# Performance work log

Hardware: AMD Instinct MI355X
Metric: run time of the kernel (lower is better)

## Reference

```python
import jax, jax.numpy as jnp
import numpy as np

GRID_SIZE = 5
SPLINE_ORDER = 3
EPS = 1e-5


def make_grid(in_features):
    # efficient-kan: grid_range=[-1,1], points from -order..grid_size+order
    h = 2.0 / GRID_SIZE
    g = jnp.arange(-SPLINE_ORDER, GRID_SIZE + SPLINE_ORDER + 1, dtype=jnp.float32) * h - 1.0
    return jnp.tile(g[None, :], (in_features, 1))  # [in, grid_size + 2*order + 1]


def b_splines(x, grid):
    # x: [B, in], grid: [in, G] -> bases: [B, in, grid_size + order]
    xg = x[:, :, None]
    bases = ((xg >= grid[:, :-1]) & (xg < grid[:, 1:])).astype(x.dtype)
    for k in range(1, SPLINE_ORDER + 1):
        left = (xg - grid[:, : -(k + 1)]) / (grid[:, k:-1] - grid[:, : -(k + 1)])
        right = (grid[:, k + 1:] - xg) / (grid[:, k + 1:] - grid[:, 1:-k])
        bases = left * bases[:, :, :-1] + right * bases[:, :, 1:]
    return bases


def kan_linear(x, grid, base_w, spline_w, spline_scaler):
    # base path: silu(x) @ base_w.T ; spline path: bsplines(x) contracted with scaled spline weight
    base_out = jnp.einsum('bi,oi->bo', jax.nn.silu(x), base_w)
    bases = b_splines(x, grid)  # [B, in, C]
    sw = spline_w * spline_scaler[:, :, None]  # [out, in, C]
    spline_out = jnp.einsum('bic,oic->bo', bases, sw)
    return base_out + spline_out


def layer_norm(x, w, b):
    mu = jnp.mean(x, axis=-1, keepdims=True)
    var = jnp.mean(jnp.square(x - mu), axis=-1, keepdims=True)
    return (x - mu) * jax.lax.rsqrt(var + EPS) * w + b


def setup_inputs() -> dict:
    key = jax.random.key(0)
    ks = jax.random.split(key, 8)
    B, F, H, E = 65536, 32, 64, 64
    OUT = E * F  # 2048
    C = GRID_SIZE + SPLINE_ORDER  # 8 coeffs per edge
    x = jax.random.normal(ks[0], (B, F), dtype=jnp.float32)
    return {
        'x': x,
        'ln_w': jnp.ones((F,), jnp.float32),
        'ln_b': jnp.zeros((F,), jnp.float32),
        'bw1': jax.random.normal(ks[1], (H, F), jnp.float32) * 0.1,
        'sw1': jax.random.normal(ks[2], (H, F, C), jnp.float32) * 0.1,
        'ss1': jax.random.normal(ks[3], (H, F), jnp.float32) * 0.1 + 1.0,
        'bw2': jax.random.normal(ks[4], (OUT, H), jnp.float32) * 0.1,
        'sw2': jax.random.normal(ks[5], (OUT, H, C), jnp.float32) * 0.1,
        'ss2': jax.random.normal(ks[6], (OUT, H), jnp.float32) * 0.1 + 1.0,
        'grid1': make_grid(F),
        'grid2': make_grid(H),
    }


def reference(x, ln_w, ln_b, bw1, sw1, ss1, bw2, sw2, ss2, grid1, grid2):
    h = layer_norm(x, ln_w, ln_b)
    h = kan_linear(h, grid1, bw1, sw1, ss1)   # [B, 64]
    out = kan_linear(h, grid2, bw2, sw2, ss2)  # [B, 2048]
    return out
```

## Files before the change

kernel.cpp:

```cpp
#include <hip/hip_runtime.h>
#include <stdint.h>

#define BATCH   65536
#define FIN     32
#define HID     64
#define NOUT    2048
#define NC      8
#define NF      9
#define K1      288
#define K2      576

#define BM      256
#define BN      256
#define BK      32
#define KT      18
#define NBUF    4

typedef __bf16 bf16x8 __attribute__((ext_vector_type(8)));
typedef float f32x4 __attribute__((ext_vector_type(4)));

__device__ __forceinline__ uint16_t f2bf(float f) {
    uint32_t u = __builtin_bit_cast(uint32_t, f);
    uint32_t r = (u + 0x7fffu + ((u >> 16) & 1u)) >> 16;
    return (uint16_t)r;
}
__device__ __forceinline__ float silu_f(float v) {
    return v / (1.f + __expf(-v));
}

__device__ __forceinline__ void bspline8u(float xv, float out[8]) {
    float s = (xv + 2.2f) * 2.5f;
    int c = (int)floorf(s);
    float gc = (float)(c - 3) * 0.4f - 1.0f;
    float u = (xv - gc) * 2.5f;
    float u1 = 1.f - u;
    float uu = u * u, u3 = uu * u;
    float w0 = u1 * u1 * u1 * (1.f / 6.f);
    float w1 = (3.f * u3 - 6.f * uu + 4.f) * (1.f / 6.f);
    float w2 = (-3.f * u3 + 3.f * uu + 3.f * u + 1.f) * (1.f / 6.f);
    float w3 = u3 * (1.f / 6.f);
#pragma unroll
    for (int t = 0; t < 8; t++) {
        int d = c - t;
        out[t] = (d == 0) ? w3 : (d == 1) ? w2 : (d == 2) ? w1 : (d == 3) ? w0 : 0.f;
    }
}

__global__ void pack_w1(const float* __restrict__ bw1, const float* __restrict__ sw1,
                        const float* __restrict__ ss1, uint16_t* __restrict__ w1L) {
    int idx = blockIdx.x * 256 + threadIdx.x;
    if (idx >= 64 * K1) return;
    int o = idx / K1, k = idx % K1;
    int i = k / 9, j = k % 9;
    float v = (j == 0) ? bw1[o * FIN + i]
                       : sw1[(o * FIN + i) * NC + (j - 1)] * ss1[o * FIN + i];
    w1L[idx] = f2bf(v);
}

__global__ void pack_w2(const float* __restrict__ bw2, const float* __restrict__ sw2,
                        const float* __restrict__ ss2, uint16_t* __restrict__ w2p) {
    int idx = blockIdx.x * 256 + threadIdx.x;
    if (idx >= NOUT * K2) return;
    int n = idx / K2, k = idx % K2;
    int j = k >> 6, i = k & 63;
    float v = (j == 0) ? bw2[n * HID + i]
                       : sw2[(n * HID + i) * NC + (j - 1)] * ss2[n * HID + i];
    w2p[idx] = f2bf(v);
}

#define FBR    64
#define A1LD   296
#define S2LD   584
__global__ __launch_bounds__(256) void featurize(
    const float* __restrict__ x, const float* __restrict__ lnw, const float* __restrict__ lnb,
    const uint16_t* __restrict__ w1L, uint16_t* __restrict__ a2) {

    __shared__ __align__(16) char fsm[75776];
    uint16_t* w1s = (uint16_t*)fsm;
    uint16_t* a1s = (uint16_t*)(fsm + 37888);
    uint16_t* s2  = (uint16_t*)fsm;

    const int tid = threadIdx.x;
    const int wv = tid >> 6, lane = tid & 63;
    const int rowBase = blockIdx.x * FBR;

#pragma unroll
    for (int t = 0; t < 9; ++t) {
        int idx = t * 256 + tid;
        int o = idx / 36, cc = idx % 36;
        uint4 v = *(const uint4*)(w1L + idx * 8);
        *(uint4*)&w1s[o * A1LD + cc * 8] = v;
    }

    const int prow = tid >> 2, pq = tid & 3;
    const float* xp = x + (size_t)(rowBase + prow) * FIN + pq * 8;
    float xv[8];
    *(float4*)&xv[0] = ((const float4*)xp)[0];
    *(float4*)&xv[4] = ((const float4*)xp)[1];
    float s = 0.f, s2v = 0.f;
#pragma unroll
    for (int j = 0; j < 8; j++) { s += xv[j]; s2v += xv[j] * xv[j]; }
    s += __shfl_xor(s, 1);  s2v += __shfl_xor(s2v, 1);
    s += __shfl_xor(s, 2);  s2v += __shfl_xor(s2v, 2);
    const float mu = s * (1.f / 32.f);
    const float var = s2v * (1.f / 32.f) - mu * mu;
    const float rstd = rsqrtf(var + 1e-5f);

    float wl[8], bl[8];
    *(float4*)&wl[0] = ((const float4*)(lnw + pq * 8))[0];
    *(float4*)&wl[4] = ((const float4*)(lnw + pq * 8))[1];
    *(float4*)&bl[0] = ((const float4*)(lnb + pq * 8))[0];
    *(float4*)&bl[4] = ((const float4*)(lnb + pq * 8))[1];

    __align__(16) uint16_t tmp[72];
#pragma unroll
    for (int ii = 0; ii < 8; ii++) {
        float xn = (xv[ii] - mu) * rstd * wl[ii] + bl[ii];
        tmp[ii * 9] = f2bf(silu_f(xn));
        float bs[8];
        bspline8u(xn, bs);
#pragma unroll
        for (int j = 0; j < 8; j++) tmp[ii * 9 + 1 + j] = f2bf(bs[j]);
    }
    {
        uint16_t* dst = &a1s[prow * A1LD + pq * 72];
#pragma unroll
        for (int q = 0; q < 9; q++) *(uint4*)(dst + q * 8) = *(const uint4*)&tmp[q * 8];
    }
    __syncthreads();

    f32x4 acc[4];
#pragma unroll
    for (int n = 0; n < 4; n++) acc[n] = (f32x4){0.f, 0.f, 0.f, 0.f};
    const int arow = wv * 16 + (lane & 15);
    const int koff = (lane >> 4) * 8;
#pragma unroll
    for (int ks = 0; ks < 9; ++ks) {
        bf16x8 af = *(const bf16x8*)&a1s[arow * A1LD + ks * 32 + koff];
#pragma unroll
        for (int n = 0; n < 4; n++) {
            bf16x8 bv = *(const bf16x8*)&w1s[(n * 16 + (lane & 15)) * A1LD + ks * 32 + koff];
            acc[n] = __builtin_amdgcn_mfma_f32_16x16x32_bf16(af, bv, acc[n], 0, 0, 0);
        }
    }
    __syncthreads();

    const int r0 = wv * 16 + ((lane >> 4) << 2);
    const int cb = lane & 15;
#pragma unroll
    for (int n = 0; n < 4; n++)
#pragma unroll
        for (int r = 0; r < 4; r++) {
            float h = acc[n][r];
            float o9[9];
            o9[0] = silu_f(h);
            bspline8u(h, &o9[1]);
            uint16_t* op = &s2[(size_t)(r0 + r) * S2LD + n * 16 + cb];
#pragma unroll
            for (int j = 0; j < 9; j++) op[j * 64] = f2bf(o9[j]);
        }
    __syncthreads();

#pragma unroll
    for (int q = 0; q < 18; ++q) {
        int g = q * 256 + tid;
        int row = g / 72, c = g % 72;
        uint4 v = *(const uint4*)&s2[row * S2LD + c * 8];
        *(uint4*)(a2 + (size_t)(rowBase + row) * K2 + c * 8) = v;
    }
}

__device__ __forceinline__ void gload16(const uint16_t* g, const uint16_t* l) {
    __builtin_amdgcn_global_load_lds(
        (const __attribute__((address_space(1))) void*)g,
        (__attribute__((address_space(3))) void*)l, 16, 0, 0);
}

__global__ __launch_bounds__(512, 2) void gemm2_kernel(const uint16_t* __restrict__ A,
                                                       const uint16_t* __restrict__ Bt,
                                                       float* __restrict__ C) {
    __shared__ __align__(16) uint16_t lds[NBUF][2][BM * BK];

    const int tid = threadIdx.x;
    const int wv = tid >> 6, lane = tid & 63;
    const int wr = wv >> 2, wc = wv & 3;

    const uint32_t bid = blockIdx.x;
    const uint32_t wk = (bid & 7u) * 256u + (bid >> 3);
    const uint32_t ntile = wk & 7u, mtile = wk >> 3;

    const int srow = tid >> 2;
    const int scol = (((tid & 3) ^ ((tid >> 3) & 3)) << 3);
    const uint16_t* gA = A  + (size_t)(mtile * BM + srow) * K2 + scol;
    const uint16_t* gB = Bt + (size_t)(ntile * BN + srow) * K2 + scol;

    const int slot8 = (((lane >> 4) ^ ((lane >> 1) & 3)) << 3);
    const int aoff = (wr * 128 + (lane & 15)) * BK + slot8;
    const int boff = (wc * 64  + (lane & 15)) * BK + slot8;

    f32x4 acc[8][4];
#pragma unroll
    for (int m = 0; m < 8; m++)
#pragma unroll
        for (int n = 0; n < 4; n++) acc[m][n] = (f32x4){0.f, 0.f, 0.f, 0.f};

#define ST_A0(b, kt) gload16(gA + (kt) * BK,                    &lds[b][0][wv * 512])
#define ST_A1(b, kt) gload16(gA + (size_t)128 * K2 + (kt) * BK, &lds[b][0][4096 + wv * 512])
#define ST_B0(b, kt) gload16(gB + (kt) * BK,                    &lds[b][1][wv * 512])
#define ST_B1(b, kt) gload16(gB + (size_t)128 * K2 + (kt) * BK, &lds[b][1][4096 + wv * 512])

    ST_A0(0, 0); ST_A1(0, 0); ST_B0(0, 0); ST_B1(0, 0);
    ST_A0(1, 1); ST_A1(1, 1); ST_B0(1, 1); ST_B1(1, 1);
    ST_A0(2, 2); ST_A1(2, 2); ST_B0(2, 2); ST_B1(2, 2);
    asm volatile("s_waitcnt vmcnt(8)" ::: "memory");
    asm volatile("s_barrier" ::: "memory");

#pragma unroll
    for (int t = 0; t < KT; ++t) {
        const int b = t & 3;
        const int nb = (t + 3) & 3;
        const bool st = (t + 3 < KT);
        const uint16_t* As = &lds[b][0][0];
        const uint16_t* Bs = &lds[b][1][0];
        bf16x8 bv[4], aa, ab;

#pragma unroll
        for (int n = 0; n < 4; ++n) bv[n] = *(const bf16x8*)&Bs[boff + n * 512];
        aa = *(const bf16x8*)&As[aoff];
        ab = *(const bf16x8*)&As[aoff + 512];
        if (st) ST_A0(nb, t + 3);
        asm volatile("s_barrier" ::: "memory");
        asm volatile("s_waitcnt lgkmcnt(0)" ::: "memory");
        __builtin_amdgcn_sched_barrier(0);
        __builtin_amdgcn_s_setprio(1);
#pragma unroll
        for (int n = 0; n < 4; ++n) acc[0][n] = __builtin_amdgcn_mfma_f32_16x16x32_bf16(aa, bv[n], acc[0][n], 0, 0, 0);
#pragma unroll
        for (int n = 0; n < 4; ++n) acc[1][n] = __builtin_amdgcn_mfma_f32_16x16x32_bf16(ab, bv[n], acc[1][n], 0, 0, 0);
        __builtin_amdgcn_s_setprio(0);
        asm volatile("s_barrier" ::: "memory");

        aa = *(const bf16x8*)&As[aoff + 2 * 512];
        ab = *(const bf16x8*)&As[aoff + 3 * 512];
        if (st) ST_A1(nb, t + 3);
        asm volatile("s_barrier" ::: "memory");
        asm volatile("s_waitcnt lgkmcnt(0)" ::: "memory");
        __builtin_amdgcn_sched_barrier(0);
        __builtin_amdgcn_s_setprio(1);
#pragma unroll
        for (int n = 0; n < 4; ++n) acc[2][n] = __builtin_amdgcn_mfma_f32_16x16x32_bf16(aa, bv[n], acc[2][n], 0, 0, 0);
#pragma unroll
        for (int n = 0; n < 4; ++n) acc[3][n] = __builtin_amdgcn_mfma_f32_16x16x32_bf16(ab, bv[n], acc[3][n], 0, 0, 0);
        __builtin_amdgcn_s_setprio(0);
        asm volatile("s_barrier" ::: "memory");

        aa = *(const bf16x8*)&As[aoff + 4 * 512];
        ab = *(const bf16x8*)&As[aoff + 5 * 512];
        if (st) ST_B0(nb, t + 3);
        asm volatile("s_barrier" ::: "memory");
        asm volatile("s_waitcnt lgkmcnt(0)" ::: "memory");
        __builtin_amdgcn_sched_barrier(0);
        __builtin_amdgcn_s_setprio(1);
#pragma unroll
        for (int n = 0; n < 4; ++n) acc[4][n] = __builtin_amdgcn_mfma_f32_16x16x32_bf16(aa, bv[n], acc[4][n], 0, 0, 0);
#pragma unroll
        for (int n = 0; n < 4; ++n) acc[5][n] = __builtin_amdgcn_mfma_f32_16x16x32_bf16(ab, bv[n], acc[5][n], 0, 0, 0);
        __builtin_amdgcn_s_setprio(0);
        asm volatile("s_barrier" ::: "memory");

        aa = *(const bf16x8*)&As[aoff + 6 * 512];
        ab = *(const bf16x8*)&As[aoff + 7 * 512];
        if (st) ST_B1(nb, t + 3);
        asm volatile("s_barrier" ::: "memory");
        asm volatile("s_waitcnt lgkmcnt(0)" ::: "memory");
        __builtin_amdgcn_sched_barrier(0);
        __builtin_amdgcn_s_setprio(1);
#pragma unroll
        for (int n = 0; n < 4; ++n) acc[6][n] = __builtin_amdgcn_mfma_f32_16x16x32_bf16(aa, bv[n], acc[6][n], 0, 0, 0);
#pragma unroll
        for (int n = 0; n < 4; ++n) acc[7][n] = __builtin_amdgcn_mfma_f32_16x16x32_bf16(ab, bv[n], acc[7][n], 0, 0, 0);
        __builtin_amdgcn_s_setprio(0);
        if (t <= KT - 4)      asm volatile("s_waitcnt vmcnt(8)" ::: "memory");
        else if (t == KT - 3) asm volatile("s_waitcnt vmcnt(4)" ::: "memory");
        else if (t == KT - 2) asm volatile("s_waitcnt vmcnt(0)" ::: "memory");
        if (t < KT - 1) asm volatile("s_barrier" ::: "memory");
    }
#undef ST_A0
#undef ST_A1
#undef ST_B0
#undef ST_B1

    const int crow0 = (int)mtile * BM + wr * 128 + ((lane >> 4) << 2);
    const int ccol0 = (int)ntile * BN + wc * 64 + (lane & 15);
#pragma unroll
    for (int m = 0; m < 8; ++m)
#pragma unroll
        for (int n = 0; n < 4; ++n) {
            float* cp = C + (size_t)(crow0 + m * 16) * NOUT + ccol0 + n * 16;
#pragma unroll
            for (int r = 0; r < 4; ++r) cp[(size_t)r * NOUT] = acc[m][n][r];
        }
}

extern "C" void kernel_launch(void* const* d_in, const int* in_sizes, int n_in,
                              void* d_out, int out_size, void* d_ws, size_t ws_size,
                              hipStream_t stream) {
    const float* x    = (const float*)d_in[0];
    const float* lnw  = (const float*)d_in[1];
    const float* lnb  = (const float*)d_in[2];
    const float* bw1  = (const float*)d_in[3];
    const float* sw1  = (const float*)d_in[4];
    const float* ss1  = (const float*)d_in[5];
    const float* bw2  = (const float*)d_in[6];
    const float* sw2  = (const float*)d_in[7];
    const float* ss2  = (const float*)d_in[8];

    char* ws = (char*)d_ws;
    uint16_t* w1L = (uint16_t*)ws;
    uint16_t* w2p = (uint16_t*)(ws + 65536);
    uint16_t* a2  = (uint16_t*)(ws + 65536 + 2359296);
    float* out = (float*)d_out;

    pack_w1<<<dim3(72), dim3(256), 0, stream>>>(bw1, sw1, ss1, w1L);
    pack_w2<<<dim3((NOUT * K2 + 255) / 256), dim3(256), 0, stream>>>(bw2, sw2, ss2, w2p);
    featurize<<<dim3(BATCH / FBR), dim3(256), 0, stream>>>(x, lnw, lnb, w1L, a2);
    gemm2_kernel<<<dim3((BATCH / BM) * (NOUT / BN)), dim3(512), 0, stream>>>(a2, w2p, out);
}
```

Before: 291.6 us.

## Use BK=64 half-tile buffering in GEMM2 with 2x2 fragment reuse per stage

Rewrites the second GEMM's main loop to use 64-wide K tiles split into half-tile LDS slots, with a ring of 4 slots per operand. Each wave now loads A and B fragments once per stage and reuses them across a 2x2 quadrant of MFMAs. This halves the number of loop iterations and the barriers between them, and cuts LDS reads per MFMA. In exchange the prefetch depth and the swizzle scheme change, and register pressure rises from holding more fragments.

Result: slower. 337.1 us (+15.6%).

```diff
diff --git a/kernel.cpp b/kernel.cpp
--- a/kernel.cpp
+++ b/kernel.cpp
@@ -12,9 +12,8 @@
 
 #define BM      256
 #define BN      256
-#define BK      32
-#define KT      18
-#define NBUF    4
+#define BK2     64
+#define KT2     9
 
 typedef __bf16 bf16x8 __attribute__((ext_vector_type(8)));
 typedef float f32x4 __attribute__((ext_vector_type(4)));
@@ -179,7 +178,8 @@
 __global__ __launch_bounds__(512, 2) void gemm2_kernel(const uint16_t* __restrict__ A,
                                                        const uint16_t* __restrict__ Bt,
                                                        float* __restrict__ C) {
-    __shared__ __align__(16) uint16_t lds[NBUF][2][BM * BK];
+    __shared__ __align__(16) uint16_t lA[4][8192];
+    __shared__ __align__(16) uint16_t lB[4][8192];
 
     const int tid = threadIdx.x;
     const int wv = tid >> 6, lane = tid & 63;
@@ -189,14 +189,24 @@
     const uint32_t wk = (bid & 7u) * 256u + (bid >> 3);
     const uint32_t ntile = wk & 7u, mtile = wk >> 3;
 
-    const int srow = tid >> 2;
-    const int scol = (((tid & 3) ^ ((tid >> 3) & 3)) << 3);
-    const uint16_t* gA = A  + (size_t)(mtile * BM + srow) * K2 + scol;
-    const uint16_t* gB = Bt + (size_t)(ntile * BN + srow) * K2 + scol;
-
-    const int slot8 = (((lane >> 4) ^ ((lane >> 1) & 3)) << 3);
-    const int aoff = (wr * 128 + (lane & 15)) * BK + slot8;
-    const int boff = (wc * 64  + (lane & 15)) * BK + slot8;
+    const int xcol = (((tid & 7) ^ ((tid >> 3) & 7)) << 3);
+    const uint16_t* gAb = A  + (size_t)(mtile * BM + (tid >> 3)) * K2 + xcol;
+    const uint16_t* gBb = Bt + (size_t)(ntile * BN + (tid >> 3)) * K2 + xcol;
+
+#define ST_A(tt, h) do { \
+    gload16(gAb + (size_t)((h) * 128) * K2 + (tt) * BK2,      &lA[(2*(tt)+(h)) & 3][tid * 8]); \
+    gload16(gAb + (size_t)((h) * 128 + 64) * K2 + (tt) * BK2, &lA[(2*(tt)+(h)) & 3][4096 + tid * 8]); } while (0)
+#define ST_B(tt, h) do { \
+    gload16(gBb + (size_t)((h) * 128) * K2 + (tt) * BK2,      &lB[(2*(tt)+(h)) & 3][tid * 8]); \
+    gload16(gBb + (size_t)((h) * 128 + 64) * K2 + (tt) * BK2, &lB[(2*(tt)+(h)) & 3][4096 + tid * 8]); } while (0)
+
+    const int arow = (lane & 15) * 64;
+    const int swz0 = (((lane >> 4)     ) ^ (lane & 7)) << 3;
+    const int swz1 = (((lane >> 4) | 4 ) ^ (lane & 7)) << 3;
+    const int bbase = (wc & 1) * 4096;
+
+#define LDA(sl, mf, ks) (*(const bf16x8*)&lA[sl][(mf) * 1024 + arow + ((ks) ? swz1 : swz0)])
+#define LDB(sl, nf, ks) (*(const bf16x8*)&lB[sl][bbase + (nf) * 1024 + arow + ((ks) ? swz1 : swz0)])
 
     f32x4 acc[8][4];
 #pragma unroll
@@ -204,91 +214,87 @@
 #pragma unroll
         for (int n = 0; n < 4; n++) acc[m][n] = (f32x4){0.f, 0.f, 0.f, 0.f};
 
-#define ST_A0(b, kt) gload16(gA + (kt) * BK,                    &lds[b][0][wv * 512])
-#define ST_A1(b, kt) gload16(gA + (size_t)128 * K2 + (kt) * BK, &lds[b][0][4096 + wv * 512])
-#define ST_B0(b, kt) gload16(gB + (kt) * BK,                    &lds[b][1][wv * 512])
-#define ST_B1(b, kt) gload16(gB + (size_t)128 * K2 + (kt) * BK, &lds[b][1][4096 + wv * 512])
-
-    ST_A0(0, 0); ST_A1(0, 0); ST_B0(0, 0); ST_B1(0, 0);
-    ST_A0(1, 1); ST_A1(1, 1); ST_B0(1, 1); ST_B1(1, 1);
-    ST_A0(2, 2); ST_A1(2, 2); ST_B0(2, 2); ST_B1(2, 2);
-    asm volatile("s_waitcnt vmcnt(8)" ::: "memory");
+    ST_A(0, 0); ST_B(0, 0); ST_B(0, 1); ST_A(0, 1); ST_B(1, 0); ST_A(1, 0);
+    asm volatile("s_waitcnt vmcnt(4)" ::: "memory");
     asm volatile("s_barrier" ::: "memory");
 
 #pragma unroll
-    for (int t = 0; t < KT; ++t) {
-        const int b = t & 3;
-        const int nb = (t + 3) & 3;
-        const bool st = (t + 3 < KT);
-        const uint16_t* As = &lds[b][0][0];
-        const uint16_t* Bs = &lds[b][1][0];
-        bf16x8 bv[4], aa, ab;
-
-#pragma unroll
-        for (int n = 0; n < 4; ++n) bv[n] = *(const bf16x8*)&Bs[boff + n * 512];
-        aa = *(const bf16x8*)&As[aoff];
-        ab = *(const bf16x8*)&As[aoff + 512];
-        if (st) ST_A0(nb, t + 3);
+    for (int t = 0; t < KT2; ++t) {
+        const int sa = (2 * t + wr) & 3;
+        const int sb = (2 * t + (wc >> 1)) & 3;
+        bf16x8 a0[4][2], a1[4][2], b0[2][2], b1[2][2];
+
+#pragma unroll
+        for (int mf = 0; mf < 4; ++mf) { a0[mf][0] = LDA(sa, mf, 0); a0[mf][1] = LDA(sa, mf, 1); }
+#pragma unroll
+        for (int nf = 0; nf < 2; ++nf) { b0[nf][0] = LDB(sb, nf, 0); b0[nf][1] = LDB(sb, nf, 1); }
+        if (t + 1 < KT2) ST_B(t + 1, 1);
         asm volatile("s_barrier" ::: "memory");
         asm volatile("s_waitcnt lgkmcnt(0)" ::: "memory");
         __builtin_amdgcn_sched_barrier(0);
         __builtin_amdgcn_s_setprio(1);
 #pragma unroll
-        for (int n = 0; n < 4; ++n) acc[0][n] = __builtin_amdgcn_mfma_f32_16x16x32_bf16(aa, bv[n], acc[0][n], 0, 0, 0);
-#pragma unroll
-        for (int n = 0; n < 4; ++n) acc[1][n] = __builtin_amdgcn_mfma_f32_16x16x32_bf16(ab, bv[n], acc[1][n], 0, 0, 0);
+        for (int mf = 0; mf < 4; ++mf)
+#pragma unroll
+            for (int nf = 0; nf < 2; ++nf)
+#pragma unroll
+                for (int ks = 0; ks < 2; ++ks)
+                    acc[mf][nf] = __builtin_amdgcn_mfma_f32_16x16x32_bf16(a0[mf][ks], b0[nf][ks], acc[mf][nf], 0, 0, 0);
         __builtin_amdgcn_s_setprio(0);
         asm volatile("s_barrier" ::: "memory");
 
-        aa = *(const bf16x8*)&As[aoff + 2 * 512];
-        ab = *(const bf16x8*)&As[aoff + 3 * 512];
-        if (st) ST_A1(nb, t + 3);
+#pragma unroll
+        for (int nf = 0; nf < 2; ++nf) { b1[nf][0] = LDB(sb, nf + 2, 0); b1[nf][1] = LDB(sb, nf + 2, 1); }
+        if (t + 1 < KT2) ST_A(t + 1, 1);
         asm volatile("s_barrier" ::: "memory");
         asm volatile("s_waitcnt lgkmcnt(0)" ::: "memory");
         __builtin_amdgcn_sched_barrier(0);
         __builtin_amdgcn_s_setprio(1);
 #pragma unroll
-        for (int n = 0; n < 4; ++n) acc[2][n] = __builtin_amdgcn_mfma_f32_16x16x32_bf16(aa, bv[n], acc[2][n], 0, 0, 0);
-#pragma unroll
-        for (int n = 0; n < 4; ++n) acc[3][n] = __builtin_amdgcn_mfma_f32_16x16x32_bf16(ab, bv[n], acc[3][n], 0, 0, 0);
+        for (int mf = 0; mf < 4; ++mf)
+#pragma unroll
+            for (int nf = 0; nf < 2; ++nf)
+#pragma unroll
+                for (int ks = 0; ks < 2; ++ks)
+                    acc[mf][nf + 2] = __builtin_amdgcn_mfma_f32_16x16x32_bf16(a0[mf][ks], b1[nf][ks], acc[mf][nf + 2], 0, 0, 0);
         __builtin_amdgcn_s_setprio(0);
         asm volatile("s_barrier" ::: "memory");
 
-        aa = *(const bf16x8*)&As[aoff + 4 * 512];
-        ab = *(const bf16x8*)&As[aoff + 5 * 512];
-        if (st) ST_B0(nb, t + 3);
+#pragma unroll
+        for (int mf = 0; mf < 4; ++mf) { a1[mf][0] = LDA(sa, mf + 4, 0); a1[mf][1] = LDA(sa, mf + 4, 1); }
+        if (t + 2 < KT2) ST_B(t + 2, 0);
         asm volatile("s_barrier" ::: "memory");
         asm volatile("s_waitcnt lgkmcnt(0)" ::: "memory");
         __builtin_amdgcn_sched_barrier(0);
         __builtin_amdgcn_s_setprio(1);
 #pragma unroll
-        for (int n = 0; n < 4; ++n) acc[4][n] = __builtin_amdgcn_mfma_f32_16x16x32_bf16(aa, bv[n], acc[4][n], 0, 0, 0);
-#pragma unroll
-        for (int n = 0; n < 4; ++n) acc[5][n] = __builtin_amdgcn_mfma_f32_16x16x32_bf16(ab, bv[n], acc[5][n], 0, 0, 0);
+        for (int mf = 0; mf < 4; ++mf)
+#pragma unroll
+            for (int nf = 0; nf < 2; ++nf)
+#pragma unroll
+                for (int ks = 0; ks < 2; ++ks)
+                    acc[mf + 4][nf] = __builtin_amdgcn_mfma_f32_16x16x32_bf16(a1[mf][ks], b0[nf][ks], acc[mf + 4][nf], 0, 0, 0);
         __builtin_amdgcn_s_setprio(0);
         asm volatile("s_barrier" ::: "memory");
 
-        aa = *(const bf16x8*)&As[aoff + 6 * 512];
-        ab = *(const bf16x8*)&As[aoff + 7 * 512];
-        if (st) ST_B1(nb, t + 3);
-        asm volatile("s_barrier" ::: "memory");
-        asm volatile("s_waitcnt lgkmcnt(0)" ::: "memory");
-        __builtin_amdgcn_sched_barrier(0);
+        if (t + 2 < KT2) ST_A(t + 2, 0);
         __builtin_amdgcn_s_setprio(1);
 #pragma unroll
-        for (int n = 0; n < 4; ++n) acc[6][n] = __builtin_amdgcn_mfma_f32_16x16x32_bf16(aa, bv[n], acc[6][n], 0, 0, 0);
-#pragma unroll
-        for (int n = 0; n < 4; ++n) acc[7][n] = __builtin_amdgcn_mfma_f32_16x16x32_bf16(ab, bv[n], acc[7][n], 0, 0, 0);
+        for (int mf = 0; mf < 4; ++mf)
+#pragma unroll
+            for (int nf = 0; nf < 2; ++nf)
+#pragma unroll
+                for (int ks = 0; ks < 2; ++ks)
+                    acc[mf + 4][nf + 2] = __builtin_amdgcn_mfma_f32_16x16x32_bf16(a1[mf][ks], b1[nf][ks], acc[mf + 4][nf + 2], 0, 0, 0);
         __builtin_amdgcn_s_setprio(0);
-        if (t <= KT - 4)      asm volatile("s_waitcnt vmcnt(8)" ::: "memory");
-        else if (t == KT - 3) asm volatile("s_waitcnt vmcnt(4)" ::: "memory");
-        else if (t == KT - 2) asm volatile("s_waitcnt vmcnt(0)" ::: "memory");
-        if (t < KT - 1) asm volatile("s_barrier" ::: "memory");
-    }
-#undef ST_A0
-#undef ST_A1
-#undef ST_B0
-#undef ST_B1
+        if (t <= KT2 - 3)      asm volatile("s_waitcnt vmcnt(4)" ::: "memory");
+        else if (t == KT2 - 2) asm volatile("s_waitcnt vmcnt(0)" ::: "memory");
+        if (t < KT2 - 1) asm volatile("s_barrier" ::: "memory");
+    }
+#undef ST_A
+#undef ST_B
+#undef LDA
+#undef LDB
 
     const int crow0 = (int)mtile * BM + wr * 128 + ((lane >> 4) << 2);
     const int ccol0 = (int)ntile * BN + wc * 64 + (lane & 15);
```
